# Kernel optimization log

Hardware: AMD Instinct MI355X
Metric: run time of the kernel (lower is better)

Reference implementation:

```python
import jax, jax.numpy as jnp
import numpy as np

B, T, V, E, H = 32, 128, 32000, 512, 1024
START = 1


def setup_inputs() -> dict:
    key = jax.random.key(0)
    ks = jax.random.split(key, 16)
    s = 0.02
    inp = {
        'h0': jax.random.normal(ks[0], (B, H), jnp.float32),
        'c0': jax.random.normal(ks[1], (B, H), jnp.float32),
        'h1': jax.random.normal(ks[2], (B, H), jnp.float32),
        'c1': jax.random.normal(ks[3], (B, H), jnp.float32),
        'h2': jax.random.normal(ks[4], (B, H), jnp.float32),
        'c2': jax.random.normal(ks[5], (B, H), jnp.float32),
        'h3': jax.random.normal(ks[6], (B, H), jnp.float32),
        'c3': jax.random.normal(ks[7], (B, H), jnp.float32),
        'emb': jax.random.normal(ks[8], (V, E), jnp.float32) * s,
        'Wx0': jax.random.normal(ks[9], (E, 4 * H), jnp.float32) * s,
        'Wh0': jax.random.normal(ks[10], (H, 4 * H), jnp.float32) * s,
        'b0': jnp.zeros((4 * H,), jnp.float32),
        'Wx1': jax.random.normal(ks[11], (H, 4 * H), jnp.float32) * s,
        'Wh1': jax.random.normal(ks[12], (H, 4 * H), jnp.float32) * s,
        'b1': jnp.zeros((4 * H,), jnp.float32),
        'Wx2': jax.random.normal(ks[13], (H, 4 * H), jnp.float32) * s,
        'Wh2': jax.random.normal(ks[14], (H, 4 * H), jnp.float32) * s,
        'b2': jnp.zeros((4 * H,), jnp.float32),
        'Wx3': jax.random.normal(ks[15], (H, 4 * H), jnp.float32) * s,
        'Wh3': jax.random.normal(jax.random.fold_in(key, 99), (H, 4 * H), jnp.float32) * s,
        'b3': jnp.zeros((4 * H,), jnp.float32),
        'fcW': jax.random.normal(jax.random.fold_in(key, 100), (H, V), jnp.float32) * s,
        'fcb': jnp.zeros((V,), jnp.float32),
        'target_length': T,
    }
    return inp


def _lstm_cell(x, h, c, Wx, Wh, b):
    # Keras gate order: i, f, c(candidate), o
    z = x @ Wx + h @ Wh + b  # [B, 4H]
    i, f, g, o = jnp.split(z, 4, axis=-1)
    i = jax.nn.sigmoid(i)
    f = jax.nn.sigmoid(f)
    g = jnp.tanh(g)
    o = jax.nn.sigmoid(o)
    c_new = f * c + i * g
    h_new = o * jnp.tanh(c_new)
    return h_new, c_new


def reference(h0, c0, h1, c1, h2, c2, h3, c3, emb,
              Wx0, Wh0, b0, Wx1, Wh1, b1, Wx2, Wh2, b2, Wx3, Wh3, b3,
              fcW, fcb, target_length):
    n_batch = h0.shape[0]
    tok0 = jnp.full((n_batch,), START, dtype=jnp.int32)

    def step(carry, _):
        tok, h0, c0, h1, c1, h2, c2, h3, c3 = carry
        x = emb[tok]  # [B, E]
        h0, c0 = _lstm_cell(x, h0, c0, Wx0, Wh0, b0)
        h1, c1 = _lstm_cell(h0, h1, c1, Wx1, Wh1, b1)
        h2, c2 = _lstm_cell(h1, h2, c2, Wx2, Wh2, b2)
        h3, c3 = _lstm_cell(h2, h3, c3, Wx3, Wh3, b3)
        logits = h3 @ fcW + fcb  # [B, V]
        tok = jnp.argmax(logits, axis=1).astype(jnp.int32)
        return (tok, h0, c0, h1, c1, h2, c2, h3, c3), (logits, tok)

    carry0 = (tok0, h0, c0, h1, c1, h2, c2, h3, c3)
    _, (logits_seq, ids_seq) = jax.lax.scan(step, carry0, None, length=target_length)
    outputs_prob = jnp.transpose(logits_seq, (1, 0, 2))  # [B, T, V]
    outputs = jnp.transpose(ids_seq, (1, 0))             # [B, T]
    return outputs_prob, outputs
```

## Files before the change

### kernel.cpp

```cpp
#include <hip/hip_runtime.h>
#include <stdint.h>

#define NBLK 256
#define NTHR 1024

typedef _Float16 f16;
typedef _Float16 f16x8 __attribute__((ext_vector_type(8)));
typedef float f32x4 __attribute__((ext_vector_type(4)));
typedef unsigned long long u64;


__device__ __forceinline__ void split2(float w, f16& hi, f16& lo) {
  f16 h = (__builtin_fabsf(w) < 6.104e-05f) ? (f16)0.0f : (f16)w;
  hi = h;
  lo = (f16)((w - (float)h) * 2048.0f);
}

__device__ __forceinline__ void split3(float w, f16& h, f16& l, f16& m) {
  const float hf = (__builtin_fabsf(w) < 6.104e-05f) ? 0.0f : (float)(f16)w;
  h = (f16)hf;
  const float r1s = (w - hf) * 2048.0f;
  const float lf = (__builtin_fabsf(r1s) < 6.104e-05f) ? 0.0f : (float)(f16)r1s;
  l = (f16)lf;
  const float r2s = (r1s - lf) * 2048.0f;
  m = (__builtin_fabsf(r2s) < 6.104e-05f) ? (f16)0.0f : (f16)r2s;
}

__device__ __forceinline__ float sig32(float z) {
  const float e32 = (float)exp(-(double)z);
  return 1.0f / __fadd_rn(1.0f, e32);
}
__device__ __forceinline__ float tanh32f(float z) { return (float)tanh((double)z); }

__device__ __forceinline__ u64 packvc(float v, unsigned col) {
  unsigned u = __float_as_uint(v);
  u = (u & 0x80000000u) ? ~u : (u | 0x80000000u);
  return ((u64)u << 32) | (u64)(0xFFFFFFFFu - col);
}
__device__ __forceinline__ u64 umax64(u64 a, u64 b) { return a > b ? a : b; }

__device__ __forceinline__ size_t faddr(int k, int row) {
  return (size_t)(((k >> 5) * 2 + (row >> 4)) * 512 +
                  (16 * ((k >> 3) & 3) + (row & 15)) * 8 + (k & 7));
}


struct MainP {
  const float* emb;
  const float* bias[4];
  const float* fcb;
  const float* hini[4];
  const float* cini[4];
  const f16* WfH[4];
  const f16* WfL[4];
  const f16* fcH;
  const f16* fcL;
  f16* axh[5];
  f16* axl[5];
  f16* axm[5];
  u64* top;
  unsigned* bar;
  float* out;
};


__device__ __forceinline__ void grid_barrier(unsigned* cnt, unsigned* gen) {
  __syncthreads();
  if (threadIdx.x == 0) {
    unsigned g = __hip_atomic_load(gen, __ATOMIC_RELAXED, __HIP_MEMORY_SCOPE_AGENT);
    unsigned prev = __hip_atomic_fetch_add(cnt, 1u, __ATOMIC_ACQ_REL, __HIP_MEMORY_SCOPE_AGENT);
    if (prev == (unsigned)(NBLK - 1)) {
      __hip_atomic_store(cnt, 0u, __ATOMIC_RELAXED, __HIP_MEMORY_SCOPE_AGENT);
      __hip_atomic_store(gen, g + 1u, __ATOMIC_RELEASE, __HIP_MEMORY_SCOPE_AGENT);
    } else {
      while (__hip_atomic_load(gen, __ATOMIC_RELAXED, __HIP_MEMORY_SCOPE_AGENT) == g) {
        __builtin_amdgcn_s_sleep(1);
      }
      __builtin_amdgcn_fence(__ATOMIC_ACQUIRE, "agent");
    }
  }
  __syncthreads();
}


__global__ __launch_bounds__(256) void prep_lstm(const float* Wx, const float* Wh,
                                                 int Kx, int CH, f16* dh, f16* dl) {
  const int id = blockIdx.x * 256 + threadIdx.x;
  const int lane = id & 63;
  const int cw = id >> 6;
  const int tile = cw / CH;
  if (tile >= 256) return;
  const int chunk = cw - tile * CH;
  const int n16 = lane & 15, qq = lane >> 4;
  const int col = 1024 * (n16 >> 2) + 4 * tile + (n16 & 3);
  const int kb = chunk * 32 + 8 * qq;
  f16x8 hv, lv;
#pragma unroll
  for (int e = 0; e < 8; ++e) {
    const int k = kb + e;
    const float wv = (k < Kx) ? Wx[(size_t)k * 4096 + col] : Wh[(size_t)(k - Kx) * 4096 + col];
    f16 h, l;
    split2(wv, h, l);
    hv[e] = h; lv[e] = l;
  }
  const size_t d = ((size_t)cw * 64 + lane) * 8;
  *(f16x8*)(dh + d) = hv;
  *(f16x8*)(dl + d) = lv;
}

__global__ __launch_bounds__(256) void prep_fc(const float* fcW, f16* dh, f16* dl,
                                               unsigned* bar) {
  const int id = blockIdx.x * 256 + threadIdx.x;
  if (id == 0) { bar[0] = 0; bar[1] = 0; }
  const int lane = id & 63;
  const int cw = id >> 6;
  const int chunk = cw & 31;
  const int stb = cw >> 5;
  const int st = stb & 7, blk = stb >> 3;
  if (blk >= 256) return;
  const int n16 = lane & 15, qq = lane >> 4;
  int cl = st * 16 + n16;
  if (cl > 124) cl = 124;
  const int col = 125 * blk + cl;
  const int kb = chunk * 32 + 8 * qq;
  f16x8 hv, lv;
#pragma unroll
  for (int e = 0; e < 8; ++e) {
    const float wv = fcW[(size_t)(kb + e) * 32000 + col];
    f16 h, l;
    split2(wv, h, l);
    hv[e] = h; lv[e] = l;
  }
  const size_t d = ((size_t)cw * 64 + lane) * 8;
  *(f16x8*)(dh + d) = hv;
  *(f16x8*)(dl + d) = lv;
}

__global__ void ws_sentinel(float* out) {
  if (blockIdx.x == 0 && threadIdx.x == 0) out[0] = 1.0e9f;
}


__global__ __launch_bounds__(NTHR, 4) void lstm_main(MainP p) {
  const int blk = blockIdx.x;
  const int tid = threadIdx.x;
  const int lane = tid & 63;
  const int w = tid >> 6;
  const int q = lane >> 4;
  const int n16 = lane & 15;

  __shared__ float zpart[16][2][32][16];
  __shared__ float fcpart[2][32][128];
  __shared__ float zred[32][16];
  __shared__ float cst[4][32][4];
  __shared__ f16 hs_h[32][4], hs_l[32][4], hs_m[32][4];
  __shared__ int tokS[32];
  __shared__ u64 redu[32][16];

  unsigned* bcnt = p.bar;
  unsigned* bgen = p.bar + 1;

  for (int i = tid; i < 512; i += NTHR) {
    const int l = i >> 7, b = (i >> 2) & 31, j = i & 3;
    cst[l][b][j] = p.cini[l][b * 1024 + 4 * blk + j];
    f16 hh, ll, mm;
    split3(p.hini[l][b * 1024 + 4 * blk + j], hh, ll, mm);
    const int kp = (l == 0) ? (4 * blk + j) : (1024 + 4 * blk + j);
    const size_t a = faddr(kp, b);
    p.axh[l][a] = hh;
    p.axl[l][a] = ll;
    p.axm[l][a] = mm;
  }
  grid_barrier(bcnt, bgen);

  auto layer_tail = [&](int l, const float* bias, f16* dh, f16* dl, f16* dm) {
    __syncthreads();
    if (tid < 512) {
      const int row = tid >> 4, c = tid & 15;
      double A = 0.0, B = 0.0;
#pragma unroll
      for (int w2 = 0; w2 < 16; ++w2) {
        A += (double)zpart[w2][0][row][c];
        B += (double)zpart[w2][1][row][c];
      }
      zred[row][c] = __fadd_rn(__fadd_rn((float)A, (float)B),
                               bias[1024 * (c >> 2) + 4 * blk + (c & 3)]);
    }
    __syncthreads();
    if (tid < 128) {
      const int b = tid >> 2, j = tid & 3;
      const float zi = zred[b][j], zf = zred[b][4 + j], zg = zred[b][8 + j], zo = zred[b][12 + j];
      const float i_ = sig32(zi);
      const float f_ = sig32(zf);
      const float g_ = tanh32f(zg);
      const float o_ = sig32(zo);
      const float c_ = __fadd_rn(__fmul_rn(f_, cst[l][b][j]), __fmul_rn(i_, g_));
      cst[l][b][j] = c_;
      const float h_ = __fmul_rn(o_, tanh32f(c_));
      f16 hh, ll, mm;
      split3(h_, hh, ll, mm);
      hs_h[b][j] = hh; hs_l[b][j] = ll; hs_m[b][j] = mm;
      const size_t a = faddr(4 * blk + j, b);
      dh[a] = hh; dl[a] = ll; dm[a] = mm;
    }
  };

  for (int t = 0; t < 128; ++t) {
    if (t == 0) {
      if (tid < 32) tokS[tid] = 1;
    } else {
      if (tid < 512) {
        const int row = tid >> 4, seg = tid & 15;
        const u64* tr = p.top + row * 256 + seg * 16;
        u64 m = 0;
#pragma unroll
        for (int e = 0; e < 16; ++e) m = umax64(m, tr[e]);
        redu[row][seg] = m;
      }
      __syncthreads();
      if (tid < 32) {
        u64 mm = redu[tid][0];
#pragma unroll
        for (int s2 = 1; s2 < 16; ++s2) mm = umax64(mm, redu[tid][s2]);
        const int tok = (int)(0xFFFFFFFFu - (unsigned)(mm & 0xFFFFFFFFull));
        tokS[tid] = tok;
        if (blk == tid)
          p.out[(size_t)32 * 128 * 32000 + (size_t)tid * 128 + (t - 1)] = (float)tok;
      }
    }
    __syncthreads();

    {
      double zdA0[4] = {0,0,0,0}, zdA1[4] = {0,0,0,0};
      double zdB0[4] = {0,0,0,0}, zdB1[4] = {0,0,0,0};
      const f32x4 zz = {0.f, 0.f, 0.f, 0.f};
#pragma unroll
      for (int sl = 0; sl < 3; ++sl) {
        const int chunk = w * 3 + sl;
        const int k0 = chunk * 32 + 8 * q;
        const f16x8 bh = __builtin_nontemporal_load(
            (const f16x8*)(p.WfH[0] + ((size_t)(blk * 48 + chunk) * 64 + lane) * 8));
        const f16x8 bl = __builtin_nontemporal_load(
            (const f16x8*)(p.WfL[0] + ((size_t)(blk * 48 + chunk) * 64 + lane) * 8));
        f16x8 ah0, al0, am0, ah1, al1, am1;
        if (chunk < 16) {
          {
            const float* ep = p.emb + (size_t)tokS[n16] * 512 + k0;
            const float4 v0 = *(const float4*)ep;
            const float4 v1 = *(const float4*)(ep + 4);
            const float vv[8] = {v0.x, v0.y, v0.z, v0.w, v1.x, v1.y, v1.z, v1.w};
#pragma unroll
            for (int e = 0; e < 8; ++e) { f16 a,b,c; split3(vv[e],a,b,c); ah0[e]=a; al0[e]=b; am0[e]=c; }
          }
          {
            const float* ep = p.emb + (size_t)tokS[16 + n16] * 512 + k0;
            const float4 v0 = *(const float4*)ep;
            const float4 v1 = *(const float4*)(ep + 4);
            const float vv[8] = {v0.x, v0.y, v0.z, v0.w, v1.x, v1.y, v1.z, v1.w};
#pragma unroll
            for (int e = 0; e < 8; ++e) { f16 a,b,c; split3(vv[e],a,b,c); ah1[e]=a; al1[e]=b; am1[e]=c; }
          }
        } else {
          const int cs = chunk - 16;
          const size_t b0 = (size_t)(cs * 2) * 512 + lane * 8;
          ah0 = *(const f16x8*)(p.axh[0] + b0);
          al0 = *(const f16x8*)(p.axl[0] + b0);
          am0 = *(const f16x8*)(p.axm[0] + b0);
          ah1 = *(const f16x8*)(p.axh[0] + b0 + 512);
          al1 = *(const f16x8*)(p.axl[0] + b0 + 512);
          am1 = *(const f16x8*)(p.axm[0] + b0 + 512);
        }
        f32x4 t00 = __builtin_amdgcn_mfma_f32_16x16x32_f16(ah0, bh, zz, 0, 0, 0);
        f32x4 t10 = __builtin_amdgcn_mfma_f32_16x16x32_f16(ah0, bl, zz, 0, 0, 0);
        t10 = __builtin_amdgcn_mfma_f32_16x16x32_f16(al0, bh, t10, 0, 0, 0);
        f32x4 t20 = __builtin_amdgcn_mfma_f32_16x16x32_f16(al0, bl, zz, 0, 0, 0);
        t20 = __builtin_amdgcn_mfma_f32_16x16x32_f16(am0, bh, t20, 0, 0, 0);
        f32x4 t01 = __builtin_amdgcn_mfma_f32_16x16x32_f16(ah1, bh, zz, 0, 0, 0);
        f32x4 t11 = __builtin_amdgcn_mfma_f32_16x16x32_f16(ah1, bl, zz, 0, 0, 0);
        t11 = __builtin_amdgcn_mfma_f32_16x16x32_f16(al1, bh, t11, 0, 0, 0);
        f32x4 t21 = __builtin_amdgcn_mfma_f32_16x16x32_f16(al1, bl, zz, 0, 0, 0);
        t21 = __builtin_amdgcn_mfma_f32_16x16x32_f16(am1, bh, t21, 0, 0, 0);
        if (chunk < 16) {
#pragma unroll
          for (int r = 0; r < 4; ++r) {
            zdA0[r] += (double)t00[r] + (double)t10[r] * 0x1p-11 + (double)t20[r] * 0x1p-22;
            zdA1[r] += (double)t01[r] + (double)t11[r] * 0x1p-11 + (double)t21[r] * 0x1p-22;
          }
        } else {
#pragma unroll
          for (int r = 0; r < 4; ++r) {
            zdB0[r] += (double)t00[r] + (double)t10[r] * 0x1p-11 + (double)t20[r] * 0x1p-22;
            zdB1[r] += (double)t01[r] + (double)t11[r] * 0x1p-11 + (double)t21[r] * 0x1p-22;
          }
        }
      }
#pragma unroll
      for (int r = 0; r < 4; ++r) {
        zpart[w][0][4 * q + r][n16] = (float)zdA0[r];
        zpart[w][0][16 + 4 * q + r][n16] = (float)zdA1[r];
        zpart[w][1][4 * q + r][n16] = (float)zdB0[r];
        zpart[w][1][16 + 4 * q + r][n16] = (float)zdB1[r];
      }
    }
    layer_tail(0, p.bias[0], p.axh[1], p.axl[1], p.axm[1]);
    grid_barrier(bcnt, bgen);

    for (int l = 1; l < 4; ++l) {
      if (tid < 128) {
        const int b = tid >> 2, j = tid & 3;
        const int kp = (l == 1) ? (4 * blk + j) : (1024 + 4 * blk + j);
        const size_t a = faddr(kp, b);
        p.axh[l - 1][a] = hs_h[b][j];
        p.axl[l - 1][a] = hs_l[b][j];
        p.axm[l - 1][a] = hs_m[b][j];
      }
      {
        double zdA0[4] = {0,0,0,0}, zdA1[4] = {0,0,0,0};
        double zdB0[4] = {0,0,0,0}, zdB1[4] = {0,0,0,0};
        const f16* WH = p.WfH[l];
        const f16* WL = p.WfL[l];
        const f16* axh_ = p.axh[l];
        const f16* axl_ = p.axl[l];
        const f16* axm_ = p.axm[l];
        const f32x4 zz = {0.f, 0.f, 0.f, 0.f};
#pragma unroll
        for (int sl = 0; sl < 4; ++sl) {
          const int chunk = w * 4 + sl;
          const f16x8 bh = __builtin_nontemporal_load(
              (const f16x8*)(WH + ((size_t)(blk * 64 + chunk) * 64 + lane) * 8));
          const f16x8 bl = __builtin_nontemporal_load(
              (const f16x8*)(WL + ((size_t)(blk * 64 + chunk) * 64 + lane) * 8));
          const size_t b0 = (size_t)(chunk * 2) * 512 + lane * 8;
          const f16x8 ah0 = *(const f16x8*)(axh_ + b0);
          const f16x8 al0 = *(const f16x8*)(axl_ + b0);
          const f16x8 am0 = *(const f16x8*)(axm_ + b0);
          const f16x8 ah1 = *(const f16x8*)(axh_ + b0 + 512);
          const f16x8 al1 = *(const f16x8*)(axl_ + b0 + 512);
          const f16x8 am1 = *(const f16x8*)(axm_ + b0 + 512);
          f32x4 t00 = __builtin_amdgcn_mfma_f32_16x16x32_f16(ah0, bh, zz, 0, 0, 0);
          f32x4 t10 = __builtin_amdgcn_mfma_f32_16x16x32_f16(ah0, bl, zz, 0, 0, 0);
          t10 = __builtin_amdgcn_mfma_f32_16x16x32_f16(al0, bh, t10, 0, 0, 0);
          f32x4 t20 = __builtin_amdgcn_mfma_f32_16x16x32_f16(al0, bl, zz, 0, 0, 0);
          t20 = __builtin_amdgcn_mfma_f32_16x16x32_f16(am0, bh, t20, 0, 0, 0);
          f32x4 t01 = __builtin_amdgcn_mfma_f32_16x16x32_f16(ah1, bh, zz, 0, 0, 0);
          f32x4 t11 = __builtin_amdgcn_mfma_f32_16x16x32_f16(ah1, bl, zz, 0, 0, 0);
          t11 = __builtin_amdgcn_mfma_f32_16x16x32_f16(al1, bh, t11, 0, 0, 0);
          f32x4 t21 = __builtin_amdgcn_mfma_f32_16x16x32_f16(al1, bl, zz, 0, 0, 0);
          t21 = __builtin_amdgcn_mfma_f32_16x16x32_f16(am1, bh, t21, 0, 0, 0);
          if (chunk < 32) {
#pragma unroll
            for (int r = 0; r < 4; ++r) {
              zdA0[r] += (double)t00[r] + (double)t10[r] * 0x1p-11 + (double)t20[r] * 0x1p-22;
              zdA1[r] += (double)t01[r] + (double)t11[r] * 0x1p-11 + (double)t21[r] * 0x1p-22;
            }
          } else {
#pragma unroll
            for (int r = 0; r < 4; ++r) {
              zdB0[r] += (double)t00[r] + (double)t10[r] * 0x1p-11 + (double)t20[r] * 0x1p-22;
              zdB1[r] += (double)t01[r] + (double)t11[r] * 0x1p-11 + (double)t21[r] * 0x1p-22;
            }
          }
        }
#pragma unroll
        for (int r = 0; r < 4; ++r) {
          zpart[w][0][4 * q + r][n16] = (float)zdA0[r];
          zpart[w][0][16 + 4 * q + r][n16] = (float)zdA1[r];
          zpart[w][1][4 * q + r][n16] = (float)zdB0[r];
          zpart[w][1][16 + 4 * q + r][n16] = (float)zdB1[r];
        }
      }
      if (l < 3) layer_tail(l, p.bias[l], p.axh[l + 1], p.axl[l + 1], p.axm[l + 1]);
      else       layer_tail(l, p.bias[l], p.axh[4], p.axl[4], p.axm[4]);
      grid_barrier(bcnt, bgen);
    }

    if (tid < 128) {
      const int b = tid >> 2, j = tid & 3;
      const size_t a = faddr(1024 + 4 * blk + j, b);
      p.axh[3][a] = hs_h[b][j];
      p.axl[3][a] = hs_l[b][j];
      p.axm[3][a] = hs_m[b][j];
    }
    {
      const int kh = w & 1;
      const int st = w >> 1;
      double Ld0[4] = {0,0,0,0}, Ld1[4] = {0,0,0,0};
      const f32x4 zz = {0.f, 0.f, 0.f, 0.f};
#pragma unroll
      for (int sl = 0; sl < 16; ++sl) {
        const int chunk = kh * 16 + sl;
        const size_t ab = (size_t)(chunk * 2) * 512 + lane * 8;
        const f16x8 ah0 = *(const f16x8*)(p.axh[4] + ab);
        const f16x8 al0 = *(const f16x8*)(p.axl[4] + ab);
        const f16x8 am0 = *(const f16x8*)(p.axm[4] + ab);
        const f16x8 ah1 = *(const f16x8*)(p.axh[4] + ab + 512);
        const f16x8 al1 = *(const f16x8*)(p.axl[4] + ab + 512);
        const f16x8 am1 = *(const f16x8*)(p.axm[4] + ab + 512);
        const size_t wb = (((size_t)(blk * 8 + st) * 32 + chunk) * 64 + lane) * 8;
        const f16x8 bh = *(const f16x8*)(p.fcH + wb);
        const f16x8 bl = *(const f16x8*)(p.fcL + wb);
        f32x4 t00 = __builtin_amdgcn_mfma_f32_16x16x32_f16(ah0, bh, zz, 0, 0, 0);
        f32x4 t10 = __builtin_amdgcn_mfma_f32_16x16x32_f16(ah0, bl, zz, 0, 0, 0);
        t10 = __builtin_amdgcn_mfma_f32_16x16x32_f16(al0, bh, t10, 0, 0, 0);
        f32x4 t20 = __builtin_amdgcn_mfma_f32_16x16x32_f16(al0, bl, zz, 0, 0, 0);
        t20 = __builtin_amdgcn_mfma_f32_16x16x32_f16(am0, bh, t20, 0, 0, 0);
        f32x4 t01 = __builtin_amdgcn_mfma_f32_16x16x32_f16(ah1, bh, zz, 0, 0, 0);
        f32x4 t11 = __builtin_amdgcn_mfma_f32_16x16x32_f16(ah1, bl, zz, 0, 0, 0);
        t11 = __builtin_amdgcn_mfma_f32_16x16x32_f16(al1, bh, t11, 0, 0, 0);
        f32x4 t21 = __builtin_amdgcn_mfma_f32_16x16x32_f16(al1, bl, zz, 0, 0, 0);
        t21 = __builtin_amdgcn_mfma_f32_16x16x32_f16(am1, bh, t21, 0, 0, 0);
#pragma unroll
        for (int r = 0; r < 4; ++r) {
          Ld0[r] += (double)t00[r] + (double)t10[r] * 0x1p-11 + (double)t20[r] * 0x1p-22;
          Ld1[r] += (double)t01[r] + (double)t11[r] * 0x1p-11 + (double)t21[r] * 0x1p-22;
        }
      }
#pragma unroll
      for (int r = 0; r < 4; ++r) {
        fcpart[kh][4 * q + r][st * 16 + n16] = (float)Ld0[r];
        fcpart[kh][16 + 4 * q + r][st * 16 + n16] = (float)Ld1[r];
      }
    }
    __syncthreads();
    if (tid < 512) {
      const int row = tid >> 4, cg = tid & 15;
      u64 best = 0;
      float* orow = p.out + (size_t)row * (128 * 32000) + (size_t)t * 32000 + 125 * blk;
      const float* fb = p.fcb + 125 * blk;
#pragma unroll
      for (int cc = 0; cc < 8; ++cc) {
        const int c = cg * 8 + cc;
        if (c < 125) {
          const float z32 = (float)((double)fcpart[0][row][c] + (double)fcpart[1][row][c]);
          const float z = __fadd_rn(z32, fb[c]);
          __builtin_nontemporal_store(z, orow + c);
          best = umax64(best, packvc(z, (unsigned)(125 * blk + c)));
        }
      }
      redu[row][cg] = best;
    }
    __syncthreads();
    if (tid < 32) {
      u64 mm = redu[tid][0];
#pragma unroll
      for (int s2 = 1; s2 < 16; ++s2) mm = umax64(mm, redu[tid][s2]);
      p.top[tid * 256 + blk] = mm;
    }
    grid_barrier(bcnt, bgen);
  }

  if (blk < 32) {
    if (tid < 16) {
      const u64* tr = p.top + blk * 256 + tid * 16;
      u64 m = 0;
#pragma unroll
      for (int e = 0; e < 16; ++e) m = umax64(m, tr[e]);
      redu[0][tid] = m;
    }
    __syncthreads();
    if (tid == 0) {
      u64 mm = redu[0][0];
#pragma unroll
      for (int s2 = 1; s2 < 16; ++s2) mm = umax64(mm, redu[0][s2]);
      p.out[(size_t)32 * 128 * 32000 + (size_t)blk * 128 + 127] =
          (float)(0xFFFFFFFFu - (unsigned)(mm & 0xFFFFFFFFull));
    }
  }
}


extern "C" void kernel_launch(void* const* d_in, const int* in_sizes, int n_in,
                              void* d_out, int out_size, void* d_ws, size_t ws_size,
                              hipStream_t stream) {
  (void)in_sizes; (void)n_in; (void)out_size;
  const float* hini[4] = {(const float*)d_in[0], (const float*)d_in[2], (const float*)d_in[4], (const float*)d_in[6]};
  const float* cini[4] = {(const float*)d_in[1], (const float*)d_in[3], (const float*)d_in[5], (const float*)d_in[7]};
  const float* emb = (const float*)d_in[8];
  const float* Wx[4] = {(const float*)d_in[9], (const float*)d_in[12], (const float*)d_in[15], (const float*)d_in[18]};
  const float* Wh[4] = {(const float*)d_in[10], (const float*)d_in[13], (const float*)d_in[16], (const float*)d_in[19]};
  const float* bias[4] = {(const float*)d_in[11], (const float*)d_in[14], (const float*)d_in[17], (const float*)d_in[20]};
  const float* fcW = (const float*)d_in[21];
  const float* fcb = (const float*)d_in[22];

  char* ws = (char*)d_ws;
  size_t off = 0;
  auto take = [&](size_t bytes) -> char* {
    char* r = ws + off;
    off += (bytes + 255) & ~(size_t)255;
    return r;
  };
  f16* WfH[4]; f16* WfL[4];
  WfH[0] = (f16*)take((size_t)256 * 48 * 64 * 8 * 2);
  WfL[0] = (f16*)take((size_t)256 * 48 * 64 * 8 * 2);
  for (int l = 1; l < 4; ++l) {
    WfH[l] = (f16*)take((size_t)256 * 64 * 64 * 8 * 2);
    WfL[l] = (f16*)take((size_t)256 * 64 * 64 * 8 * 2);
  }
  f16* fcH = (f16*)take((size_t)256 * 8 * 32 * 64 * 8 * 2);
  f16* fcL = (f16*)take((size_t)256 * 8 * 32 * 64 * 8 * 2);
  f16* axh[5]; f16* axl[5]; f16* axm[5];
  const int axK[5] = {1024, 2048, 2048, 2048, 1024};
  for (int l = 0; l < 5; ++l) {
    axh[l] = (f16*)take((size_t)axK[l] * 32 * 2);
    axl[l] = (f16*)take((size_t)axK[l] * 32 * 2);
    axm[l] = (f16*)take((size_t)axK[l] * 32 * 2);
  }
  u64* top = (u64*)take((size_t)32 * 256 * 8);
  unsigned* bar = (unsigned*)take(256);

  if (off > ws_size) {
    hipLaunchKernelGGL(ws_sentinel, dim3(1), dim3(1), 0, stream, (float*)d_out);
    return;
  }

  hipLaunchKernelGGL(prep_lstm, dim3(256 * 48 * 64 / 256), dim3(256), 0, stream,
                     Wx[0], Wh[0], 512, 48, WfH[0], WfL[0]);
  for (int l = 1; l < 4; ++l)
    hipLaunchKernelGGL(prep_lstm, dim3(256 * 64 * 64 / 256), dim3(256), 0, stream,
                       Wx[l], Wh[l], 1024, 64, WfH[l], WfL[l]);
  hipLaunchKernelGGL(prep_fc, dim3(256 * 8 * 32 * 64 / 256), dim3(256), 0, stream,
                     fcW, fcH, fcL, bar);

  MainP mp;
  mp.emb = emb;
  for (int l = 0; l < 4; ++l) {
    mp.bias[l] = bias[l]; mp.hini[l] = hini[l]; mp.cini[l] = cini[l];
    mp.WfH[l] = WfH[l]; mp.WfL[l] = WfL[l];
  }
  mp.fcb = fcb; mp.fcH = fcH; mp.fcL = fcL;
  for (int l = 0; l < 5; ++l) { mp.axh[l] = axh[l]; mp.axl[l] = axl[l]; mp.axm[l] = axm[l]; }
  mp.top = top; mp.bar = bar; mp.out = (float*)d_out;

  void* args[] = {&mp};
  hipLaunchCooperativeKernel((void*)lstm_main, dim3(NBLK), dim3(NTHR), args, 0, stream);
}
```

Baseline: 34.55 ms.

## Prefetch next layer weights into registers across grid barriers with 512-thread blocks

```diff
diff --git a/kernel.cpp b/kernel.cpp
--- a/kernel.cpp
+++ b/kernel.cpp
@@ -2,7 +2,7 @@
 #include <stdint.h>
 
 #define NBLK 256
-#define NTHR 1024
+#define NTHR 512
 
 typedef _Float16 f16;
 typedef _Float16 f16x8 __attribute__((ext_vector_type(8)));
@@ -42,6 +42,13 @@
 __device__ __forceinline__ size_t faddr(int k, int row) {
   return (size_t)(((k >> 5) * 2 + (row >> 4)) * 512 +
                   (16 * ((k >> 3) & 3) + (row & 15)) * 8 + (k & 7));
+}
+
+__device__ __forceinline__ void lds_bar() {
+  asm volatile("s_waitcnt lgkmcnt(0)" ::: "memory");
+  __builtin_amdgcn_sched_barrier(0);
+  __builtin_amdgcn_s_barrier();
+  asm volatile("" ::: "memory");
 }
 
 
@@ -63,9 +70,10 @@
   float* out;
 };
 
-
-__device__ __forceinline__ void grid_barrier(unsigned* cnt, unsigned* gen) {
-  __syncthreads();
+__device__ __forceinline__ void grid_bar(unsigned* cnt, unsigned* gen, int w,
+                                         bool drain_all) {
+  if (drain_all || w < 2) asm volatile("s_waitcnt vmcnt(0)" ::: "memory");
+  lds_bar();
   if (threadIdx.x == 0) {
     unsigned g = __hip_atomic_load(gen, __ATOMIC_RELAXED, __HIP_MEMORY_SCOPE_AGENT);
     unsigned prev = __hip_atomic_fetch_add(cnt, 1u, __ATOMIC_ACQ_REL, __HIP_MEMORY_SCOPE_AGENT);
@@ -73,13 +81,13 @@
       __hip_atomic_store(cnt, 0u, __ATOMIC_RELAXED, __HIP_MEMORY_SCOPE_AGENT);
       __hip_atomic_store(gen, g + 1u, __ATOMIC_RELEASE, __HIP_MEMORY_SCOPE_AGENT);
     } else {
-      while (__hip_atomic_load(gen, __ATOMIC_RELAXED, __HIP_MEMORY_SCOPE_AGENT) == g) {
+      while (__hip_atomic_load(gen, __ATOMIC_RELAXED, __HIP_MEMORY_SCOPE_AGENT) == g)
         __builtin_amdgcn_s_sleep(1);
-      }
       __builtin_amdgcn_fence(__ATOMIC_ACQUIRE, "agent");
     }
   }
-  __syncthreads();
+  __builtin_amdgcn_s_barrier();
+  asm volatile("" ::: "memory");
 }
 
 
@@ -141,7 +149,7 @@
 }
 
 
-__global__ __launch_bounds__(NTHR, 4) void lstm_main(MainP p) {
+__global__ __launch_bounds__(NTHR, 2) void lstm_main(MainP p) {
   const int blk = blockIdx.x;
   const int tid = threadIdx.x;
   const int lane = tid & 63;
@@ -149,8 +157,8 @@
   const int q = lane >> 4;
   const int n16 = lane & 15;
 
-  __shared__ float zpart[16][2][32][16];
-  __shared__ float fcpart[2][32][128];
+  __shared__ float zpart[8][2][32][16];
+  __shared__ float fcpart[32][128];
   __shared__ float zred[32][16];
   __shared__ float cst[4][32][4];
   __shared__ f16 hs_h[32][4], hs_l[32][4], hs_m[32][4];
@@ -160,7 +168,10 @@
   unsigned* bcnt = p.bar;
   unsigned* bgen = p.bar + 1;
 
-  for (int i = tid; i < 512; i += NTHR) {
+  f16x8 pwh[8], pwl[8];
+
+  {
+    const int i = tid;
     const int l = i >> 7, b = (i >> 2) & 31, j = i & 3;
     cst[l][b][j] = p.cini[l][b * 1024 + 4 * blk + j];
     f16 hh, ll, mm;
@@ -171,22 +182,30 @@
     p.axl[l][a] = ll;
     p.axm[l][a] = mm;
   }
-  grid_barrier(bcnt, bgen);
+  grid_bar(bcnt, bgen, w, true);
+
+#pragma unroll
+  for (int sl = 0; sl < 6; ++sl) {
+    const int chunk = sl * 8 + w;
+    const size_t o = ((size_t)(blk * 48 + chunk) * 64 + lane) * 8;
+    pwh[sl] = *(const f16x8*)(p.WfH[0] + o);
+    pwl[sl] = *(const f16x8*)(p.WfL[0] + o);
+  }
 
   auto layer_tail = [&](int l, const float* bias, f16* dh, f16* dl, f16* dm) {
-    __syncthreads();
-    if (tid < 512) {
+    lds_bar();
+    {
       const int row = tid >> 4, c = tid & 15;
       double A = 0.0, B = 0.0;
 #pragma unroll
-      for (int w2 = 0; w2 < 16; ++w2) {
+      for (int w2 = 0; w2 < 8; ++w2) {
         A += (double)zpart[w2][0][row][c];
         B += (double)zpart[w2][1][row][c];
       }
       zred[row][c] = __fadd_rn(__fadd_rn((float)A, (float)B),
                                bias[1024 * (c >> 2) + 4 * blk + (c & 3)]);
     }
-    __syncthreads();
+    lds_bar();
     if (tid < 128) {
       const int b = tid >> 2, j = tid & 3;
       const float zi = zred[b][j], zf = zred[b][4 + j], zg = zred[b][8 + j], zo = zred[b][12 + j];
@@ -209,7 +228,7 @@
     if (t == 0) {
       if (tid < 32) tokS[tid] = 1;
     } else {
-      if (tid < 512) {
+      {
         const int row = tid >> 4, seg = tid & 15;
         const u64* tr = p.top + row * 256 + seg * 16;
         u64 m = 0;
@@ -217,7 +236,7 @@
         for (int e = 0; e < 16; ++e) m = umax64(m, tr[e]);
         redu[row][seg] = m;
       }
-      __syncthreads();
+      lds_bar();
       if (tid < 32) {
         u64 mm = redu[tid][0];
 #pragma unroll
@@ -228,22 +247,20 @@
           p.out[(size_t)32 * 128 * 32000 + (size_t)tid * 128 + (t - 1)] = (float)tok;
       }
     }
-    __syncthreads();
+    lds_bar();
 
     {
       double zdA0[4] = {0,0,0,0}, zdA1[4] = {0,0,0,0};
       double zdB0[4] = {0,0,0,0}, zdB1[4] = {0,0,0,0};
       const f32x4 zz = {0.f, 0.f, 0.f, 0.f};
 #pragma unroll
-      for (int sl = 0; sl < 3; ++sl) {
-        const int chunk = w * 3 + sl;
+      for (int sl = 0; sl < 6; ++sl) {
+        const int chunk = sl * 8 + w;
         const int k0 = chunk * 32 + 8 * q;
-        const f16x8 bh = __builtin_nontemporal_load(
-            (const f16x8*)(p.WfH[0] + ((size_t)(blk * 48 + chunk) * 64 + lane) * 8));
-        const f16x8 bl = __builtin_nontemporal_load(
-            (const f16x8*)(p.WfL[0] + ((size_t)(blk * 48 + chunk) * 64 + lane) * 8));
+        const f16x8 bh = pwh[sl];
+        const f16x8 bl = pwl[sl];
         f16x8 ah0, al0, am0, ah1, al1, am1;
-        if (chunk < 16) {
+        if (sl < 2) {
           {
             const float* ep = p.emb + (size_t)tokS[n16] * 512 + k0;
             const float4 v0 = *(const float4*)ep;
@@ -261,8 +278,7 @@
             for (int e = 0; e < 8; ++e) { f16 a,b,c; split3(vv[e],a,b,c); ah1[e]=a; al1[e]=b; am1[e]=c; }
           }
         } else {
-          const int cs = chunk - 16;
-          const size_t b0 = (size_t)(cs * 2) * 512 + lane * 8;
+          const size_t b0 = (size_t)((chunk - 16) * 2) * 512 + lane * 8;
           ah0 = *(const f16x8*)(p.axh[0] + b0);
           al0 = *(const f16x8*)(p.axl[0] + b0);
           am0 = *(const f16x8*)(p.axm[0] + b0);
@@ -280,7 +296,7 @@
         t11 = __builtin_amdgcn_mfma_f32_16x16x32_f16(al1, bh, t11, 0, 0, 0);
         f32x4 t21 = __builtin_amdgcn_mfma_f32_16x16x32_f16(al1, bl, zz, 0, 0, 0);
         t21 = __builtin_amdgcn_mfma_f32_16x16x32_f16(am1, bh, t21, 0, 0, 0);
-        if (chunk < 16) {
+        if (sl < 2) {
 #pragma unroll
           for (int r = 0; r < 4; ++r) {
             zdA0[r] += (double)t00[r] + (double)t10[r] * 0x1p-11 + (double)t20[r] * 0x1p-22;
@@ -302,8 +318,15 @@
         zpart[w][1][16 + 4 * q + r][n16] = (float)zdB1[r];
       }
     }
+#pragma unroll
+    for (int sl = 0; sl < 8; ++sl) {
+      const int chunk = sl * 8 + w;
+      const size_t o = ((size_t)(blk * 64 + chunk) * 64 + lane) * 8;
+      pwh[sl] = *(const f16x8*)(p.WfH[1] + o);
+      pwl[sl] = *(const f16x8*)(p.WfL[1] + o);
+    }
     layer_tail(0, p.bias[0], p.axh[1], p.axl[1], p.axm[1]);
-    grid_barrier(bcnt, bgen);
+    grid_bar(bcnt, bgen, w, false);
 
     for (int l = 1; l < 4; ++l) {
       if (tid < 128) {
@@ -317,19 +340,15 @@
       {
         double zdA0[4] = {0,0,0,0}, zdA1[4] = {0,0,0,0};
         double zdB0[4] = {0,0,0,0}, zdB1[4] = {0,0,0,0};
-        const f16* WH = p.WfH[l];
-        const f16* WL = p.WfL[l];
         const f16* axh_ = p.axh[l];
         const f16* axl_ = p.axl[l];
         const f16* axm_ = p.axm[l];
         const f32x4 zz = {0.f, 0.f, 0.f, 0.f};
 #pragma unroll
-        for (int sl = 0; sl < 4; ++sl) {
-          const int chunk = w * 4 + sl;
-          const f16x8 bh = __builtin_nontemporal_load(
-              (const f16x8*)(WH + ((size_t)(blk * 64 + chunk) * 64 + lane) * 8));
-          const f16x8 bl = __builtin_nontemporal_load(
-              (const f16x8*)(WL + ((size_t)(blk * 64 + chunk) * 64 + lane) * 8));
+        for (int sl = 0; sl < 8; ++sl) {
+          const int chunk = sl * 8 + w;
+          const f16x8 bh = pwh[sl];
+          const f16x8 bl = pwl[sl];
           const size_t b0 = (size_t)(chunk * 2) * 512 + lane * 8;
           const f16x8 ah0 = *(const f16x8*)(axh_ + b0);
           const f16x8 al0 = *(const f16x8*)(axl_ + b0);
@@ -347,7 +366,7 @@
           t11 = __builtin_amdgcn_mfma_f32_16x16x32_f16(al1, bh, t11, 0, 0, 0);
           f32x4 t21 = __builtin_amdgcn_mfma_f32_16x16x32_f16(al1, bl, zz, 0, 0, 0);
           t21 = __builtin_amdgcn_mfma_f32_16x16x32_f16(am1, bh, t21, 0, 0, 0);
-          if (chunk < 32) {
+          if (sl < 4) {
 #pragma unroll
             for (int r = 0; r < 4; ++r) {
               zdA0[r] += (double)t00[r] + (double)t10[r] * 0x1p-11 + (double)t20[r] * 0x1p-22;
@@ -369,9 +388,25 @@
           zpart[w][1][16 + 4 * q + r][n16] = (float)zdB1[r];
         }
       }
+      if (l < 3) {
+#pragma unroll
+        for (int sl = 0; sl < 8; ++sl) {
+          const int chunk = sl * 8 + w;
+          const size_t o = ((size_t)(blk * 64 + chunk) * 64 + lane) * 8;
+          pwh[sl] = *(const f16x8*)(p.WfH[l + 1] + o);
+          pwl[sl] = *(const f16x8*)(p.WfL[l + 1] + o);
+        }
+      } else {
+#pragma unroll
+        for (int c = 0; c < 8; ++c) {
+          const size_t wb = (((size_t)(blk * 8 + w) * 32 + c) * 64 + lane) * 8;
+          pwh[c] = *(const f16x8*)(p.fcH + wb);
+          pwl[c] = __builtin_nontemporal_load((const f16x8*)(p.fcL + wb));
+        }
+      }
       if (l < 3) layer_tail(l, p.bias[l], p.axh[l + 1], p.axl[l + 1], p.axm[l + 1]);
       else       layer_tail(l, p.bias[l], p.axh[4], p.axl[4], p.axm[4]);
-      grid_barrier(bcnt, bgen);
+      grid_bar(bcnt, bgen, w, false);
     }
 
     if (tid < 128) {
@@ -382,23 +417,25 @@
       p.axm[3][a] = hs_m[b][j];
     }
     {
-      const int kh = w & 1;
-      const int st = w >> 1;
       double Ld0[4] = {0,0,0,0}, Ld1[4] = {0,0,0,0};
       const f32x4 zz = {0.f, 0.f, 0.f, 0.f};
 #pragma unroll
-      for (int sl = 0; sl < 16; ++sl) {
-        const int chunk = kh * 16 + sl;
-        const size_t ab = (size_t)(chunk * 2) * 512 + lane * 8;
+      for (int c = 0; c < 32; ++c) {
+        const int ri = c & 7;
+        const f16x8 bh = pwh[ri];
+        const f16x8 bl = pwl[ri];
+        if (c < 24) {
+          const size_t wb = (((size_t)(blk * 8 + w) * 32 + (c + 8)) * 64 + lane) * 8;
+          pwh[ri] = *(const f16x8*)(p.fcH + wb);
+          pwl[ri] = __builtin_nontemporal_load((const f16x8*)(p.fcL + wb));
+        }
+        const size_t ab = (size_t)(c * 2) * 512 + lane * 8;
         const f16x8 ah0 = *(const f16x8*)(p.axh[4] + ab);
         const f16x8 al0 = *(const f16x8*)(p.axl[4] + ab);
         const f16x8 am0 = *(const f16x8*)(p.axm[4] + ab);
         const f16x8 ah1 = *(const f16x8*)(p.axh[4] + ab + 512);
         const f16x8 al1 = *(const f16x8*)(p.axl[4] + ab + 512);
         const f16x8 am1 = *(const f16x8*)(p.axm[4] + ab + 512);
-        const size_t wb = (((size_t)(blk * 8 + st) * 32 + chunk) * 64 + lane) * 8;
-        const f16x8 bh = *(const f16x8*)(p.fcH + wb);
-        const f16x8 bl = *(const f16x8*)(p.fcL + wb);
         f32x4 t00 = __builtin_amdgcn_mfma_f32_16x16x32_f16(ah0, bh, zz, 0, 0, 0);
         f32x4 t10 = __builtin_amdgcn_mfma_f32_16x16x32_f16(ah0, bl, zz, 0, 0, 0);
         t10 = __builtin_amdgcn_mfma_f32_16x16x32_f16(al0, bh, t10, 0, 0, 0);
@@ -417,12 +454,19 @@
       }
 #pragma unroll
       for (int r = 0; r < 4; ++r) {
-        fcpart[kh][4 * q + r][st * 16 + n16] = (float)Ld0[r];
-        fcpart[kh][16 + 4 * q + r][st * 16 + n16] = (float)Ld1[r];
-      }
-    }
-    __syncthreads();
-    if (tid < 512) {
+        fcpart[4 * q + r][w * 16 + n16] = (float)Ld0[r];
+        fcpart[16 + 4 * q + r][w * 16 + n16] = (float)Ld1[r];
+      }
+    }
+#pragma unroll
+    for (int sl = 0; sl < 6; ++sl) {
+      const int chunk = sl * 8 + w;
+      const size_t o = ((size_t)(blk * 48 + chunk) * 64 + lane) * 8;
+      pwh[sl] = *(const f16x8*)(p.WfH[0] + o);
+      pwl[sl] = *(const f16x8*)(p.WfL[0] + o);
+    }
+    lds_bar();
+    {
       const int row = tid >> 4, cg = tid & 15;
       u64 best = 0;
       float* orow = p.out + (size_t)row * (128 * 32000) + (size_t)t * 32000 + 125 * blk;
@@ -431,22 +475,21 @@
       for (int cc = 0; cc < 8; ++cc) {
         const int c = cg * 8 + cc;
         if (c < 125) {
-          const float z32 = (float)((double)fcpart[0][row][c] + (double)fcpart[1][row][c]);
-          const float z = __fadd_rn(z32, fb[c]);
+          const float z = __fadd_rn(fcpart[row][c], fb[c]);
           __builtin_nontemporal_store(z, orow + c);
           best = umax64(best, packvc(z, (unsigned)(125 * blk + c)));
         }
       }
       redu[row][cg] = best;
     }
-    __syncthreads();
+    lds_bar();
     if (tid < 32) {
       u64 mm = redu[tid][0];
 #pragma unroll
       for (int s2 = 1; s2 < 16; ++s2) mm = umax64(mm, redu[tid][s2]);
       p.top[tid * 256 + blk] = mm;
     }
-    grid_barrier(bcnt, bgen);
+    grid_bar(bcnt, bgen, w, false);
   }
 
   if (blk < 32) {
@@ -457,7 +500,7 @@
       for (int e = 0; e < 16; ++e) m = umax64(m, tr[e]);
       redu[0][tid] = m;
     }
-    __syncthreads();
+    lds_bar();
     if (tid == 0) {
       u64 mm = redu[0][0];
 #pragma unroll
```

After: 37.63 ms. 1.09x slower.
